# Performance work log

Hardware: AMD Instinct MI355X
Metric: run time of the kernel (lower is better)

The kernel has to match this reference:

```python
import jax, jax.numpy as jnp
import numpy as np

M = 12          # persons per frame
K = 2           # partition channels from conv1da (1024 = 2*512)
D = 512         # GCN channel dim / LSTM hidden
C_IN = 4096     # backbone feature dim
NUM_CLASSES = 8


def setup_inputs() -> dict:
    key = jax.random.key(0)
    ks = jax.random.split(key, 8)
    N, T = 16, 32
    NT = N * T
    base_out = jax.random.normal(ks[0], (NT, M, C_IN), dtype=jnp.float32)
    dist = jax.random.uniform(ks[1], (N, T, 3, K, M, M), dtype=jnp.float32)
    # conv1da: Conv1d(4096 -> 1024, k=1, bias=False) == matmul with [1024, 4096]
    w_a = jax.random.normal(ks[2], (K * D, C_IN), dtype=jnp.float32) * 0.02
    # LSTM(512, 512, 1): torch gate order i, f, g, o
    s = 1.0 / np.sqrt(D)
    w_ih = jax.random.uniform(ks[3], (4 * D, D), minval=-s, maxval=s, dtype=jnp.float32)
    w_hh = jax.random.uniform(ks[4], (4 * D, D), minval=-s, maxval=s, dtype=jnp.float32)
    b_ih = jax.random.uniform(ks[5], (4 * D,), minval=-s, maxval=s, dtype=jnp.float32)
    b_hh = jax.random.uniform(ks[6], (4 * D,), minval=-s, maxval=s, dtype=jnp.float32)
    # gclassifier: Linear(512 -> num_classes)
    w_cls = jax.random.normal(ks[7], (NUM_CLASSES, D), dtype=jnp.float32) * 0.01
    b_cls = jnp.zeros((NUM_CLASSES,), dtype=jnp.float32)
    return {"base_out": base_out, "dist": dist, "w_a": w_a,
            "w_ih": w_ih, "w_hh": w_hh, "b_ih": b_ih, "b_hh": b_hh,
            "w_cls": w_cls, "b_cls": b_cls, "n_videos": N}


def reference(base_out, dist, w_a, w_ih, w_hh, b_ih, b_hh, w_cls, b_cls, n_videos):
    NT = base_out.shape[0]
    N = n_videos
    T = NT // N
    # conv1da (1x1 conv, no bias): [NT, M, 4096] -> [NT, K*D, M] -> [NT, K, D, M]
    node1 = jnp.einsum('nmc,oc->nom', base_out, w_a).reshape(NT, K, D, M)
    # fused three-way adjacency aggregation: node1a + node1b + node1c
    A = (dist[:, :, 2] + dist[:, :, 1] + dist[:, :, 0]).reshape(NT, K, M, M)
    node = jnp.einsum('nkcv,nkvw->ncw', node1, A)  # [NT, D, M]
    node = jax.nn.relu(node)
    # AdaptiveAvgPool1d(1) over the M persons
    pooled = node.mean(axis=2)                      # [NT, D]
    seq = pooled.reshape(N, T, D)
    # torch nn.LSTM default batch_first=False: iterates over axis 0 (N), batch=T
    def step(carry, x_t):
        h, c = carry
        g = x_t @ w_ih.T + b_ih + h @ w_hh.T + b_hh  # [T, 4D]
        i, f, gg, o = jnp.split(g, 4, axis=-1)
        c = jax.nn.sigmoid(f) * c + jax.nn.sigmoid(i) * jnp.tanh(gg)
        h = jax.nn.sigmoid(o) * jnp.tanh(c)
        return (h, c), h
    h0 = jnp.zeros((T, D), dtype=seq.dtype)
    c0 = jnp.zeros((T, D), dtype=seq.dtype)
    _, hs = jax.lax.scan(step, (h0, c0), seq)       # [N, T, D]
    last = hs[:, -1, :]                              # video_feat[:, -1, :]
    return last @ w_cls.T + b_cls                    # [N, num_classes]
```

## Files before the change

### kernel.cpp

```cpp
#include <hip/hip_runtime.h>
#include <math.h>

#define MM 12
#define KK 2
#define DD 512
#define CIN 4096
#define NCLS 8
#define NV 16
#define TT 32

typedef unsigned long long u64;
typedef __attribute__((ext_vector_type(8))) __bf16 bf16x8;
typedef __attribute__((ext_vector_type(4))) float f32x4;

#define PART_F   0
#define POOLED_F 786432
#define TAGGX_F  794752
#define HGLOB_F  796800
#define GX_F     813184
#define PART_KS_STRIDE (192 * 1024)

#define MFMA_BF16(A, B, C) __builtin_amdgcn_mfma_f32_16x16x32_bf16((A), (B), (C), 0, 0, 0)
#define LOADR(p)      __hip_atomic_load((p), __ATOMIC_RELAXED, __HIP_MEMORY_SCOPE_AGENT)
#define LOADACQ(p)    __hip_atomic_load((p), __ATOMIC_ACQUIRE, __HIP_MEMORY_SCOPE_AGENT)
#define STOREREL(p, v) __hip_atomic_store((p), (v), __ATOMIC_RELEASE, __HIP_MEMORY_SCOPE_AGENT)
#define LOADS(p)      __hip_atomic_load((p), __ATOMIC_RELAXED, __HIP_MEMORY_SCOPE_SYSTEM)
#define EXCHS(p, v)   (void)__hip_atomic_exchange((p), (v), __ATOMIC_RELAXED, __HIP_MEMORY_SCOPE_SYSTEM)

static __device__ __forceinline__ u64 ld_sc0(const u64* p) {
  u64 v;
  asm volatile("global_load_dwordx2 %0, %1, off sc0\n\ts_waitcnt vmcnt(0)"
               : "=v"(v) : "v"(p) : "memory");
  return v;
}
static __device__ __forceinline__ void st_sc0(u64* p, u64 v) {
  asm volatile("global_store_dwordx2 %0, %1, off sc0" :: "v"(p), "v"(v) : "memory");
}

static __device__ __forceinline__ void cvt_store(
    unsigned short* __restrict__ hb, unsigned short* __restrict__ lb,
    int idx, float4 v) {
  unsigned ux = __float_as_uint(v.x), uy = __float_as_uint(v.y);
  unsigned uz = __float_as_uint(v.z), uw = __float_as_uint(v.w);
  *(uint2*)&hb[idx] = make_uint2((ux >> 16) | (uy & 0xFFFF0000u),
                                 (uz >> 16) | (uw & 0xFFFF0000u));
  unsigned lx = __float_as_uint(v.x - __uint_as_float(ux & 0xFFFF0000u));
  unsigned ly = __float_as_uint(v.y - __uint_as_float(uy & 0xFFFF0000u));
  unsigned lz = __float_as_uint(v.z - __uint_as_float(uz & 0xFFFF0000u));
  unsigned lw = __float_as_uint(v.w - __uint_as_float(uw & 0xFFFF0000u));
  *(uint2*)&lb[idx] = make_uint2((lx >> 16) | (ly & 0xFFFF0000u),
                                 (lz >> 16) | (lw & 0xFFFF0000u));
}

__global__ __launch_bounds__(64, 1) void k_gemm(
    const float* __restrict__ base_out, const float* __restrict__ w_a,
    float* __restrict__ part)
{
  const int wg = blockIdx.x;
  const int ks = wg & 3;
  const int ot = (wg >> 2) & 63;
  const int jq = (wg >> 8) & 3;
  const int cc0 = ks * 1024;
  const int lane = threadIdx.x;

  __shared__ __align__(16) unsigned short Ah[16 * 40], Al[16 * 40];
  __shared__ __align__(16) unsigned short Bh[48 * 40], Bl[48 * 40];

  const int sq = lane & 7;
  const int sr = lane >> 3;

  unsigned boff[6];
#pragma unroll
  for (int rep = 0; rep < 6; ++rep) {
    const int jl = sr + 8 * rep;
    const int j = jq * 48 + jl;
    const int n = j / 12, m = j - n * 12;
    boff[rep] = (unsigned)(((n * TT + 31) * MM + m) * CIN + cc0 + sq * 4);
  }
  unsigned aoff[2];
#pragma unroll
  for (int repA = 0; repA < 2; ++repA)
    aoff[repA] = (unsigned)((ot * 16 + sr + 8 * repA) * CIN + cc0 + sq * 4);

  f32x4 acc0 = {0.f, 0.f, 0.f, 0.f}, acc1 = acc0, acc2 = acc0;

  float4 pa[2], pb[6];
#pragma unroll
  for (int repA = 0; repA < 2; ++repA) pa[repA] = *(const float4*)&w_a[aoff[repA]];
#pragma unroll
  for (int rep = 0; rep < 6; ++rep) pb[rep] = *(const float4*)&base_out[boff[rep]];

  for (int st = 0; st < 32; ++st) {
#pragma unroll
    for (int repA = 0; repA < 2; ++repA)
      cvt_store(Ah, Al, (sr + 8 * repA) * 40 + sq * 4, pa[repA]);
#pragma unroll
    for (int rep = 0; rep < 6; ++rep)
      cvt_store(Bh, Bl, (sr + 8 * rep) * 40 + sq * 4, pb[rep]);
    if (st < 31) {
#pragma unroll
      for (int repA = 0; repA < 2; ++repA) {
        aoff[repA] += 32;
        pa[repA] = *(const float4*)&w_a[aoff[repA]];
      }
#pragma unroll
      for (int rep = 0; rep < 6; ++rep) {
        boff[rep] += 32;
        pb[rep] = *(const float4*)&base_out[boff[rep]];
      }
    }
    const int koff = (lane >> 4) * 8;
    const int fra = (lane & 15) * 40 + koff;
    bf16x8 oh = *(const bf16x8*)&Ah[fra];
    bf16x8 ol = *(const bf16x8*)&Al[fra];
    {
      const int r0 = (0 * 16 + (lane & 15)) * 40 + koff;
      bf16x8 jh = *(const bf16x8*)&Bh[r0], jl = *(const bf16x8*)&Bl[r0];
      acc0 = MFMA_BF16(jh, oh, acc0);
      acc0 = MFMA_BF16(jh, ol, acc0);
      acc0 = MFMA_BF16(jl, oh, acc0);
    }
    {
      const int r1 = (1 * 16 + (lane & 15)) * 40 + koff;
      bf16x8 jh = *(const bf16x8*)&Bh[r1], jl = *(const bf16x8*)&Bl[r1];
      acc1 = MFMA_BF16(jh, oh, acc1);
      acc1 = MFMA_BF16(jh, ol, acc1);
      acc1 = MFMA_BF16(jl, oh, acc1);
    }
    {
      const int r2 = (2 * 16 + (lane & 15)) * 40 + koff;
      bf16x8 jh = *(const bf16x8*)&Bh[r2], jl = *(const bf16x8*)&Bl[r2];
      acc2 = MFMA_BF16(jh, oh, acc2);
      acc2 = MFMA_BF16(jh, ol, acc2);
      acc2 = MFMA_BF16(jl, oh, acc2);
    }
  }
  const int o = ot * 16 + (lane & 15);
  const int jr = (lane >> 4) * 4;
#pragma unroll
  for (int r = 0; r < 4; ++r) {
    part[((size_t)ks * 192 + jq * 48 + 0 * 16 + jr + r) * 1024 + o] = acc0[r];
    part[((size_t)ks * 192 + jq * 48 + 1 * 16 + jr + r) * 1024 + o] = acc1[r];
    part[((size_t)ks * 192 + jq * 48 + 2 * 16 + jr + r) * 1024 + o] = acc2[r];
  }
}

__global__ __launch_bounds__(256, 1) void k_pool(
    const float* __restrict__ dist, const float* __restrict__ part,
    float* __restrict__ pooled)
{
  const int wg = blockIdx.x;
  const int tid = threadIdx.x;

  __shared__ float Asum_s[KK * MM * MM];

  const int n = wg >> 4, cb = (wg & 15) * 32;
  const unsigned dbase = (unsigned)((n * TT + 31) * (3 * KK * MM * MM));
  for (int f = tid; f < KK * MM * MM; f += 256)
    Asum_s[f] = dist[dbase + f] + dist[dbase + KK * MM * MM + f]
              + dist[dbase + 2 * KK * MM * MM + f];
  __syncthreads();
  if (tid < 32) {
    const int c = cb + tid;
    float nd[KK][MM];
#pragma unroll
    for (int k = 0; k < KK; ++k)
#pragma unroll
      for (int v = 0; v < MM; ++v) {
        const size_t off = (size_t)(n * MM + v) * 1024 + k * DD + c;
        nd[k][v] = part[off] + part[off + PART_KS_STRIDE]
                 + part[off + 2 * PART_KS_STRIDE] + part[off + 3 * PART_KS_STRIDE];
      }
    float accm = 0.f;
#pragma unroll
    for (int w = 0; w < MM; ++w) {
      float sw = 0.f;
#pragma unroll
      for (int k = 0; k < KK; ++k)
#pragma unroll
        for (int v = 0; v < MM; ++v) sw += nd[k][v] * Asum_s[(k * MM + v) * MM + w];
      accm += fmaxf(sw, 0.f);
    }
    pooled[n * DD + c] = accm * (1.f / 12.f);
  }
}

__global__ __launch_bounds__(1024, 1) void k_rest(
    const float* __restrict__ pooled,
    const float* __restrict__ w_ih, const float* __restrict__ w_hh,
    const float* __restrict__ b_ih, const float* __restrict__ b_hh,
    const float* __restrict__ w_cls, const float* __restrict__ b_cls,
    unsigned* __restrict__ tagGX, float* __restrict__ gxg,
    u64* __restrict__ hg64, float* __restrict__ out)
{
  const int wg = blockIdx.x;
  const int tid = threadIdx.x;

  __shared__ __align__(16) float whh_s[64][516];
  __shared__ float gx_s[16][64];
  __shared__ __align__(16) float h_s[DD];
  __shared__ float dot_s[64];

  if ((wg & 7) != 0) {
    const int k = wg & 7;
    if (k > 4) return;
    const int m = wg >> 3;
    const int dd = m + 32 * (k - 1);
    if (tid < 256) {
      const int n = tid & 15, j = tid >> 4;
      const int gr = dd * 16 + j;
      const float4* wr = (const float4*)&w_ih[(size_t)gr * DD];
      const float4* pv = (const float4*)&pooled[(size_t)n * DD];
      float a = 0.f;
#pragma unroll 8
      for (int q = 0; q < DD / 4; ++q) {
        float4 x = wr[q], y = pv[q];
        a += x.x * y.x + x.y * y.y + x.z * y.z + x.w * y.w;
      }
      gxg[m * 1024 + n * 64 + (k - 1) * 16 + j] = a + b_ih[gr] + b_hh[gr];
    }
    __syncthreads();
    if (tid == 0) STOREREL(&tagGX[dd * 16], 1u);
    return;
  }

  const int w = wg >> 3;

  for (int f = tid; f < 64 * 128; f += 1024) {
    const int rr = f >> 7, c4 = (f & 127) * 4;
    const int grow = (rr >> 4) * DD + w * 16 + (rr & 15);
    *(float4*)&whh_s[rr][c4] = *(const float4*)&w_hh[(size_t)grow * DD + c4];
  }
  if (tid < 64) {
    bool done;
    do {
      int t0 = (int)LOADR(&tagGX[(w + 32 * (tid & 3)) * 16]);
      done = __all(t0 == 1);
    } while (!done);
  }
  __syncthreads();
  gx_s[tid >> 6][tid & 63] =
      __uint_as_float(LOADS((const unsigned*)&gxg[w * 1024 + tid]));
  __syncthreads();

  {
    float c_reg = 0.f;
    const int r = tid >> 4;
    const int lj = tid & 15;

    for (int s = 0; s < NV; ++s) {
      if (s == 0) {
        if (tid < DD) h_s[tid] = 0.f;
      } else {
        if (tid < DD) {
          const u64* p = &hg64[(size_t)(s - 1) * DD + tid];
          u64 v = ld_sc0(p);
          while ((unsigned)v != (unsigned)s) {
            v = LOADS(p);
            if ((unsigned)v == (unsigned)s) break;
            v = ld_sc0(p);
          }
          h_s[tid] = __uint_as_float((unsigned)(v >> 32));
        }
      }
      __syncthreads();

      float p = 0.f;
      const float4* wrow = (const float4*)&whh_s[r][0];
      const float4* hv4 = (const float4*)h_s;
#pragma unroll
      for (int q = 0; q < 8; ++q) {
        float4 wv = wrow[lj + 16 * q];
        float4 hv = hv4[lj + 16 * q];
        p += wv.x * hv.x + wv.y * hv.y + wv.z * hv.z + wv.w * hv.w;
      }
#pragma unroll
      for (int off = 8; off; off >>= 1) p += __shfl_down(p, off, 16);
      if (lj == 0) dot_s[r] = p;
      __syncthreads();

      if (tid < 16) {
        const float pi = gx_s[s][tid]      + dot_s[tid];
        const float pf = gx_s[s][16 + tid] + dot_s[16 + tid];
        const float pg = gx_s[s][32 + tid] + dot_s[32 + tid];
        const float po = gx_s[s][48 + tid] + dot_s[48 + tid];
        const float si = 1.f / (1.f + expf(-pi));
        const float sf = 1.f / (1.f + expf(-pf));
        const float so = 1.f / (1.f + expf(-po));
        c_reg = sf * c_reg + si * tanhf(pg);
        const float hn = so * tanhf(c_reg);
        const u64 pk = ((u64)__float_as_uint(hn) << 32) | (u64)(unsigned)(s + 1);
        u64* pp = &hg64[(size_t)s * DD + w * 16 + tid];
        st_sc0(pp, pk);
        EXCHS(pp, pk);
      }
    }
  }

  if (wg == 0) {
    float* scratch = &whh_s[0][0];
    if (tid < DD) {
      u64 vv[NV];
#pragma unroll
      for (int n = 0; n < NV; ++n) vv[n] = LOADS(&hg64[(size_t)n * DD + tid]);
#pragma unroll
      for (int n = 0; n < NV; ++n) {
        u64 v = vv[n];
        while ((unsigned)v != (unsigned)(n + 1))
          v = LOADS(&hg64[(size_t)n * DD + tid]);
        scratch[n * 516 + tid] = __uint_as_float((unsigned)(v >> 32));
      }
    }
    __syncthreads();
    if (tid < NV * NCLS) {
      const int n = tid >> 3, cl = tid & 7;
      const float4* hv = (const float4*)&scratch[n * 516];
      const float4* wv = (const float4*)(w_cls + (size_t)cl * DD);
      float a = b_cls[cl];
#pragma unroll 8
      for (int q = 0; q < DD / 4; ++q) {
        float4 x = hv[q], y = wv[q];
        a += x.x * y.x + x.y * y.y + x.z * y.z + x.w * y.w;
      }
      out[tid] = a;
    }
  }
}

extern "C" void kernel_launch(void* const* d_in, const int* in_sizes, int n_in,
                              void* d_out, int out_size, void* d_ws, size_t ws_size,
                              hipStream_t stream) {
  const float* base_out = (const float*)d_in[0];
  const float* dist     = (const float*)d_in[1];
  const float* w_a      = (const float*)d_in[2];
  const float* w_ih     = (const float*)d_in[3];
  const float* w_hh     = (const float*)d_in[4];
  const float* b_ih     = (const float*)d_in[5];
  const float* b_hh     = (const float*)d_in[6];
  const float* w_cls    = (const float*)d_in[7];
  const float* b_cls    = (const float*)d_in[8];
  float* out = (float*)d_out;

  float* ws = (float*)d_ws;
  float* part   = ws + PART_F;
  float* pooled = ws + POOLED_F;
  unsigned* tagGX = (unsigned*)(ws + TAGGX_F);
  u64* hg64 = (u64*)(ws + HGLOB_F);
  float* gxg = ws + GX_F;

  k_gemm<<<dim3(1024), 64, 0, stream>>>(base_out, w_a, part);
  k_pool<<<dim3(256), 256, 0, stream>>>(dist, part, pooled);
  k_rest<<<dim3(256), 1024, 0, stream>>>(pooled, w_ih, w_hh, b_ih, b_hh,
                                         w_cls, b_cls, tagGX, gxg, hg64, out);
}
```

Before: 260.6 us.

## Double-buffer GEMM register prefetch and move LSTM gate reduction to wave shuffles

The conv GEMM loop now keeps two register sets of prefetched tiles and is unrolled by two, so global loads are issued further ahead of their use. In the LSTM recurrence, rows are remapped so that each wave holds the i, f, g and o dot products for one hidden unit. The gate values are then gathered with cross-lane shuffles instead of through a shared-memory dot_s array plus an extra barrier, so one thread per wave computes the cell update. This removes one __syncthreads and the LDS round trip from each serial step, and adds more register pressure in the GEMM.

```diff
diff --git a/kernel.cpp b/kernel.cpp
--- a/kernel.cpp
+++ b/kernel.cpp
@@ -84,57 +84,81 @@
 
   f32x4 acc0 = {0.f, 0.f, 0.f, 0.f}, acc1 = acc0, acc2 = acc0;
 
-  float4 pa[2], pb[6];
-#pragma unroll
-  for (int repA = 0; repA < 2; ++repA) pa[repA] = *(const float4*)&w_a[aoff[repA]];
-#pragma unroll
-  for (int rep = 0; rep < 6; ++rep) pb[rep] = *(const float4*)&base_out[boff[rep]];
-
-  for (int st = 0; st < 32; ++st) {
-#pragma unroll
-    for (int repA = 0; repA < 2; ++repA)
-      cvt_store(Ah, Al, (sr + 8 * repA) * 40 + sq * 4, pa[repA]);
-#pragma unroll
-    for (int rep = 0; rep < 6; ++rep)
-      cvt_store(Bh, Bl, (sr + 8 * rep) * 40 + sq * 4, pb[rep]);
-    if (st < 31) {
-#pragma unroll
-      for (int repA = 0; repA < 2; ++repA) {
-        aoff[repA] += 32;
-        pa[repA] = *(const float4*)&w_a[aoff[repA]];
-      }
-#pragma unroll
-      for (int rep = 0; rep < 6; ++rep) {
-        boff[rep] += 32;
-        pb[rep] = *(const float4*)&base_out[boff[rep]];
-      }
-    }
-    const int koff = (lane >> 4) * 8;
-    const int fra = (lane & 15) * 40 + koff;
-    bf16x8 oh = *(const bf16x8*)&Ah[fra];
-    bf16x8 ol = *(const bf16x8*)&Al[fra];
-    {
-      const int r0 = (0 * 16 + (lane & 15)) * 40 + koff;
-      bf16x8 jh = *(const bf16x8*)&Bh[r0], jl = *(const bf16x8*)&Bl[r0];
-      acc0 = MFMA_BF16(jh, oh, acc0);
-      acc0 = MFMA_BF16(jh, ol, acc0);
-      acc0 = MFMA_BF16(jl, oh, acc0);
-    }
-    {
-      const int r1 = (1 * 16 + (lane & 15)) * 40 + koff;
-      bf16x8 jh = *(const bf16x8*)&Bh[r1], jl = *(const bf16x8*)&Bl[r1];
-      acc1 = MFMA_BF16(jh, oh, acc1);
-      acc1 = MFMA_BF16(jh, ol, acc1);
-      acc1 = MFMA_BF16(jl, oh, acc1);
-    }
-    {
-      const int r2 = (2 * 16 + (lane & 15)) * 40 + koff;
-      bf16x8 jh = *(const bf16x8*)&Bh[r2], jl = *(const bf16x8*)&Bl[r2];
-      acc2 = MFMA_BF16(jh, oh, acc2);
-      acc2 = MFMA_BF16(jh, ol, acc2);
-      acc2 = MFMA_BF16(jl, oh, acc2);
-    }
-  }
+  float4 pa0[2], pb0[6], pa1[2], pb1[6];
+#pragma unroll
+  for (int repA = 0; repA < 2; ++repA) pa0[repA] = *(const float4*)&w_a[aoff[repA]];
+#pragma unroll
+  for (int rep = 0; rep < 6; ++rep) pb0[rep] = *(const float4*)&base_out[boff[rep]];
+#pragma unroll
+  for (int repA = 0; repA < 2; ++repA) {
+    aoff[repA] += 32; pa1[repA] = *(const float4*)&w_a[aoff[repA]];
+  }
+#pragma unroll
+  for (int rep = 0; rep < 6; ++rep) {
+    boff[rep] += 32; pb1[rep] = *(const float4*)&base_out[boff[rep]];
+  }
+
+#define STAGE_SET(PA, PB)                                                   \
+  {                                                                         \
+    _Pragma("unroll")                                                       \
+    for (int repA = 0; repA < 2; ++repA)                                    \
+      cvt_store(Ah, Al, (sr + 8 * repA) * 40 + sq * 4, PA[repA]);           \
+    _Pragma("unroll")                                                       \
+    for (int rep = 0; rep < 6; ++rep)                                       \
+      cvt_store(Bh, Bl, (sr + 8 * rep) * 40 + sq * 4, PB[rep]);             \
+  }
+#define LOAD_SET(PA, PB)                                                    \
+  {                                                                         \
+    _Pragma("unroll")                                                       \
+    for (int repA = 0; repA < 2; ++repA) {                                  \
+      aoff[repA] += 32; PA[repA] = *(const float4*)&w_a[aoff[repA]];        \
+    }                                                                       \
+    _Pragma("unroll")                                                       \
+    for (int rep = 0; rep < 6; ++rep) {                                     \
+      boff[rep] += 32; PB[rep] = *(const float4*)&base_out[boff[rep]];      \
+    }                                                                       \
+  }
+#define MFMA_STEP()                                                         \
+  {                                                                         \
+    const int koff = (lane >> 4) * 8;                                       \
+    const int fra = (lane & 15) * 40 + koff;                                \
+    bf16x8 oh = *(const bf16x8*)&Ah[fra];                                   \
+    bf16x8 ol = *(const bf16x8*)&Al[fra];                                   \
+    {                                                                       \
+      const int r0 = (0 * 16 + (lane & 15)) * 40 + koff;                    \
+      bf16x8 jh = *(const bf16x8*)&Bh[r0], jl = *(const bf16x8*)&Bl[r0];    \
+      acc0 = MFMA_BF16(jh, oh, acc0);                                       \
+      acc0 = MFMA_BF16(jh, ol, acc0);                                       \
+      acc0 = MFMA_BF16(jl, oh, acc0);                                       \
+    }                                                                       \
+    {                                                                       \
+      const int r1 = (1 * 16 + (lane & 15)) * 40 + koff;                    \
+      bf16x8 jh = *(const bf16x8*)&Bh[r1], jl = *(const bf16x8*)&Bl[r1];    \
+      acc1 = MFMA_BF16(jh, oh, acc1);                                       \
+      acc1 = MFMA_BF16(jh, ol, acc1);                                       \
+      acc1 = MFMA_BF16(jl, oh, acc1);                                       \
+    }                                                                       \
+    {                                                                       \
+      const int r2 = (2 * 16 + (lane & 15)) * 40 + koff;                    \
+      bf16x8 jh = *(const bf16x8*)&Bh[r2], jl = *(const bf16x8*)&Bl[r2];    \
+      acc2 = MFMA_BF16(jh, oh, acc2);                                       \
+      acc2 = MFMA_BF16(jh, ol, acc2);                                       \
+      acc2 = MFMA_BF16(jl, oh, acc2);                                       \
+    }                                                                       \
+  }
+
+  for (int st = 0; st < 32; st += 2) {
+    STAGE_SET(pa0, pb0);
+    if (st + 2 < 32) LOAD_SET(pa0, pb0);
+    MFMA_STEP();
+    STAGE_SET(pa1, pb1);
+    if (st + 3 < 32) LOAD_SET(pa1, pb1);
+    MFMA_STEP();
+  }
+#undef STAGE_SET
+#undef LOAD_SET
+#undef MFMA_STEP
+
   const int o = ot * 16 + (lane & 15);
   const int jr = (lane >> 4) * 4;
 #pragma unroll
@@ -199,7 +223,6 @@
   __shared__ __align__(16) float whh_s[64][516];
   __shared__ float gx_s[16][64];
   __shared__ __align__(16) float h_s[DD];
-  __shared__ float dot_s[64];
 
   if ((wg & 7) != 0) {
     const int k = wg & 7;
@@ -244,9 +267,11 @@
   __syncthreads();
 
   {
+    const int wave = tid >> 6;
+    const int lane = tid & 63;
+    const int lj = lane & 15;
+    const int rl = (lane >> 4) * 16 + wave;
     float c_reg = 0.f;
-    const int r = tid >> 4;
-    const int lj = tid & 15;
 
     for (int s = 0; s < NV; ++s) {
       if (s == 0) {
@@ -266,7 +291,7 @@
       __syncthreads();
 
       float p = 0.f;
-      const float4* wrow = (const float4*)&whh_s[r][0];
+      const float4* wrow = (const float4*)&whh_s[rl][0];
       const float4* hv4 = (const float4*)h_s;
 #pragma unroll
       for (int q = 0; q < 8; ++q) {
@@ -276,24 +301,26 @@
       }
 #pragma unroll
       for (int off = 8; off; off >>= 1) p += __shfl_down(p, off, 16);
-      if (lj == 0) dot_s[r] = p;
-      __syncthreads();
-
-      if (tid < 16) {
-        const float pi = gx_s[s][tid]      + dot_s[tid];
-        const float pf = gx_s[s][16 + tid] + dot_s[16 + tid];
-        const float pg = gx_s[s][32 + tid] + dot_s[32 + tid];
-        const float po = gx_s[s][48 + tid] + dot_s[48 + tid];
+      const float df = __shfl(p, 16, 64);
+      const float dg = __shfl(p, 32, 64);
+      const float do_ = __shfl(p, 48, 64);
+      if (lane == 0) {
+        const int d = wave;
+        const float pi = gx_s[s][d]      + p;
+        const float pf = gx_s[s][16 + d] + df;
+        const float pg = gx_s[s][32 + d] + dg;
+        const float po = gx_s[s][48 + d] + do_;
         const float si = 1.f / (1.f + expf(-pi));
         const float sf = 1.f / (1.f + expf(-pf));
         const float so = 1.f / (1.f + expf(-po));
         c_reg = sf * c_reg + si * tanhf(pg);
         const float hn = so * tanhf(c_reg);
         const u64 pk = ((u64)__float_as_uint(hn) << 32) | (u64)(unsigned)(s + 1);
-        u64* pp = &hg64[(size_t)s * DD + w * 16 + tid];
+        u64* pp = &hg64[(size_t)s * DD + w * 16 + d];
         st_sc0(pp, pk);
         EXCHS(pp, pk);
       }
+      __syncthreads();
     }
   }
 
```

New measurement: 334.1 us. +28.2%, slower.
